# Kernel tuning notes

Measured on AMD Instinct MI355X. Metric: run time of the kernel, lower is better.

The kernel has to match this reference:

```python
import jax, jax.numpy as jnp
import numpy as np

B, H, L, D, S = 4, 16, 4096, 64, 128

def setup_inputs() -> dict:
    key = jax.random.key(0)
    k1, k2 = jax.random.split(key)
    x = jax.random.normal(k1, (B, H, L, D), dtype=jnp.float32)
    c = jax.random.normal(k2, (H, S, D), dtype=jnp.float32)
    # codebook rows are unit-normalized at init (matches torch init)
    c = c / jnp.linalg.norm(c, axis=-1, keepdims=True)
    return {"x": x, "c": c}

def reference(x, c):
    # cosine-similarity scores: [B,H,L,S]
    cos_sim = jnp.einsum('bhld,hsd->bhls', x, c)
    delta_index = jnp.argmax(cos_sim, axis=-1)            # [B,H,L]
    delta_onehot = jax.nn.one_hot(delta_index, c.shape[-2], dtype=jnp.float32)  # [B,H,L,S]
    return (delta_onehot, c)
```

## Files before the change

kernel.cpp:

```cpp
#include <hip/hip_runtime.h>
#include <hip/hip_bf16.h>
#include <math.h>

constexpr int BB = 4;
constexpr int HH = 16;
constexpr int LL = 4096;
constexpr int DD = 64;
constexpr int SS = 128;

constexpr int BM = 128;
constexpr int PP = 17;

__global__ __launch_bounds__(256) void quantizer_kernel(
    const float* __restrict__ x,
    const float* __restrict__ c,
    float* __restrict__ out,
    float* __restrict__ out_c)
{
    __shared__ float xs[DD * BM];
    __shared__ float cs[DD * SS];
    __shared__ int amax[BM];

    const int tid = threadIdx.x;
    const int blk = blockIdx.x;
    const long long r0 = (long long)blk * BM;
    const int h = (int)((r0 >> 12) & (HH - 1));
    const float* __restrict__ chead = c + (size_t)h * SS * DD;

    {
        const float4* __restrict__ xg = (const float4*)(x + (size_t)r0 * DD);
        const float4* __restrict__ cg = (const float4*)chead;
        #pragma unroll
        for (int it = 0; it < 8; ++it) {
            const int idx = tid + it * 256;
            const int row = idx & 127;
            const int d4  = idx >> 7;
            float4 v = xg[row * 16 + d4];
            xs[(4 * d4 + 0) * BM + row] = v.x;
            xs[(4 * d4 + 1) * BM + row] = v.y;
            xs[(4 * d4 + 2) * BM + row] = v.z;
            xs[(4 * d4 + 3) * BM + row] = v.w;
            float4 w = cg[row * 16 + d4];
            cs[(4 * d4 + 0) * SS + row] = w.x;
            cs[(4 * d4 + 1) * SS + row] = w.y;
            cs[(4 * d4 + 2) * SS + row] = w.z;
            cs[(4 * d4 + 3) * SS + row] = w.w;
        }
    }
    __syncthreads();

    const int m0 = tid >> 4;
    const int n0 = tid & 15;

    float acc[8][8] = {};

    #pragma unroll 2
    for (int k = 0; k < DD; ++k) {
        const float4 xa = *(const float4*)&xs[k * BM + m0 * 8];
        const float4 xb = *(const float4*)&xs[k * BM + m0 * 8 + 4];
        const float4 ca = *(const float4*)&cs[k * SS + n0 * 8];
        const float4 cb = *(const float4*)&cs[k * SS + n0 * 8 + 4];
        const float xv[8] = {xa.x, xa.y, xa.z, xa.w, xb.x, xb.y, xb.z, xb.w};
        const float cv[8] = {ca.x, ca.y, ca.z, ca.w, cb.x, cb.y, cb.z, cb.w};
        #pragma unroll
        for (int i = 0; i < 8; ++i)
            #pragma unroll
            for (int j = 0; j < 8; ++j)
                acc[i][j] = fmaf(xv[i], cv[j], acc[i][j]);
    }

    __syncthreads();
    float* pval = xs;
    int*   pidx = (int*)(xs + BM * PP);

    #pragma unroll
    for (int i = 0; i < 8; ++i) {
        float bv = acc[i][0];
        int bj = 0;
        #pragma unroll
        for (int j = 1; j < 8; ++j)
            if (acc[i][j] > bv) { bv = acc[i][j]; bj = j; }
        const int row = m0 * 8 + i;
        pval[row * PP + n0] = bv;
        pidx[row * PP + n0] = n0 * 8 + bj;
    }
    __syncthreads();

    if (tid < BM) {
        float bv = pval[tid * PP];
        int bi = pidx[tid * PP];
        #pragma unroll
        for (int t = 1; t < 16; ++t) {
            const float v = pval[tid * PP + t];
            const int ix = pidx[tid * PP + t];
            if (v > bv) { bv = v; bi = ix; }
        }
        amax[tid] = bi;
    }
    __syncthreads();

    float4* __restrict__ op = (float4*)(out + (size_t)r0 * SS);
    #pragma unroll 4
    for (int i = tid; i < BM * (SS / 4); i += 256) {
        const int rr = i >> 5;
        const int s0 = (i & 31) * 4;
        const int am = amax[rr];
        float4 v;
        v.x = (s0 + 0 == am) ? 1.f : 0.f;
        v.y = (s0 + 1 == am) ? 1.f : 0.f;
        v.z = (s0 + 2 == am) ? 1.f : 0.f;
        v.w = (s0 + 3 == am) ? 1.f : 0.f;
        op[i] = v;
    }

    if (blk < 128) {
        const float4* __restrict__ src = (const float4*)c;
        float4* __restrict__ dst = (float4*)out_c;
        const int idx = blk * 256 + tid;
        dst[idx] = src[idx];
    }
}

extern "C" void kernel_launch(void* const* d_in, const int* in_sizes, int n_in,
                              void* d_out, int out_size, void* d_ws, size_t ws_size,
                              hipStream_t stream) {
    const float* x = (const float*)d_in[0];
    const float* c = (const float*)d_in[1];
    float* out = (float*)d_out;
    float* out_c = out + (size_t)BB * HH * LL * SS;

    const int rows = BB * HH * LL;
    const int blocks = rows / BM;
    quantizer_kernel<<<blocks, 256, 0, stream>>>(x, c, out, out_c);
}
```

Before: 209.0 us.

## Use split-bf16 MFMA for scores with exact fp32 fallback for near ties

Replaces the fp32 FMA outer-product GEMM with bf16 MFMA 16x16x32. Each operand is split into a high and a low bf16 part and three cross products are summed to approximate fp32. Each row tracks its top-2 scores. Rows whose margin falls below a tolerance are flagged and rescored exactly in fp32 from global memory, which preserves argmax correctness. This offloads the compute to matrix cores, but adds a swizzled LDS layout, conversion overhead, and a serial per-flagged-row fallback loop with block-wide syncs.

```diff
diff --git a/kernel.cpp b/kernel.cpp
--- a/kernel.cpp
+++ b/kernel.cpp
@@ -1,5 +1,4 @@
 #include <hip/hip_runtime.h>
-#include <hip/hip_bf16.h>
 #include <math.h>
 
 constexpr int BB = 4;
@@ -7,9 +6,31 @@
 constexpr int LL = 4096;
 constexpr int DD = 64;
 constexpr int SS = 128;
-
 constexpr int BM = 128;
-constexpr int PP = 17;
+
+constexpr float TAU = 2e-3f;
+
+typedef __attribute__((ext_vector_type(8))) short bf16x8;
+typedef __attribute__((ext_vector_type(4))) float f32x4;
+
+#define MFMA16 __builtin_amdgcn_mfma_f32_16x16x32_bf16
+
+__device__ __forceinline__ unsigned short f2bf(float v) {
+    unsigned u = __float_as_uint(v);
+    return (unsigned short)((u + 0x7fffu + ((u >> 16) & 1u)) >> 16);
+}
+__device__ __forceinline__ float bf2f(unsigned short b) {
+    return __uint_as_float(((unsigned)b) << 16);
+}
+__device__ __forceinline__ unsigned swz(unsigned a) {
+    return a ^ (((a >> 8) & 3u) << 5);
+}
+__device__ __forceinline__ void st8(unsigned char* s, unsigned a, uint2 d) {
+    *(uint2*)(s + swz(a)) = d;
+}
+__device__ __forceinline__ bf16x8 ld8(const unsigned char* s, unsigned a) {
+    return *(const bf16x8*)(s + swz(a));
+}
 
 __global__ __launch_bounds__(256) void quantizer_kernel(
     const float* __restrict__ x,
@@ -17,9 +38,11 @@
     float* __restrict__ out,
     float* __restrict__ out_c)
 {
-    __shared__ float xs[DD * BM];
-    __shared__ float cs[DD * SS];
+    __shared__ __align__(16) unsigned char smem[65536];
     __shared__ int amax[BM];
+    __shared__ int s_nflag;
+    __shared__ int s_flag[BM];
+    __shared__ float s_fsc[SS];
 
     const int tid = threadIdx.x;
     const int blk = blockIdx.x;
@@ -27,77 +50,164 @@
     const int h = (int)((r0 >> 12) & (HH - 1));
     const float* __restrict__ chead = c + (size_t)h * SS * DD;
 
+    if (tid == 0) s_nflag = 0;
+
     {
         const float4* __restrict__ xg = (const float4*)(x + (size_t)r0 * DD);
         const float4* __restrict__ cg = (const float4*)chead;
         #pragma unroll
         for (int it = 0; it < 8; ++it) {
-            const int idx = tid + it * 256;
-            const int row = idx & 127;
-            const int d4  = idx >> 7;
-            float4 v = xg[row * 16 + d4];
-            xs[(4 * d4 + 0) * BM + row] = v.x;
-            xs[(4 * d4 + 1) * BM + row] = v.y;
-            xs[(4 * d4 + 2) * BM + row] = v.z;
-            xs[(4 * d4 + 3) * BM + row] = v.w;
-            float4 w = cg[row * 16 + d4];
-            cs[(4 * d4 + 0) * SS + row] = w.x;
-            cs[(4 * d4 + 1) * SS + row] = w.y;
-            cs[(4 * d4 + 2) * SS + row] = w.z;
-            cs[(4 * d4 + 3) * SS + row] = w.w;
+            const int idx = it * 256 + tid;
+            const int d4  = idx & 15;
+            const int row = idx >> 4;
+            const int kt  = d4 >> 3;
+            const int lsl = ((((d4 & 7) >> 1) << 4) | (row & 15));
+            const int boff = (d4 & 1) * 8;
+            const int t8  = row >> 4;
+            const unsigned bhi =
+                (unsigned)((((kt << 3) | t8) << 10) + lsl * 16 + boff);
+            const unsigned blo = bhi + (16u << 10);
+            {
+                float4 v = xg[idx];
+                unsigned short h0 = f2bf(v.x), h1 = f2bf(v.y),
+                               h2 = f2bf(v.z), h3 = f2bf(v.w);
+                unsigned short l0 = f2bf(v.x - bf2f(h0)),
+                               l1 = f2bf(v.y - bf2f(h1)),
+                               l2 = f2bf(v.z - bf2f(h2)),
+                               l3 = f2bf(v.w - bf2f(h3));
+                st8(smem, bhi, make_uint2((unsigned)h0 | ((unsigned)h1 << 16),
+                                          (unsigned)h2 | ((unsigned)h3 << 16)));
+                st8(smem, blo, make_uint2((unsigned)l0 | ((unsigned)l1 << 16),
+                                          (unsigned)l2 | ((unsigned)l3 << 16)));
+            }
+            {
+                float4 v = cg[idx];
+                unsigned short h0 = f2bf(v.x), h1 = f2bf(v.y),
+                               h2 = f2bf(v.z), h3 = f2bf(v.w);
+                unsigned short l0 = f2bf(v.x - bf2f(h0)),
+                               l1 = f2bf(v.y - bf2f(h1)),
+                               l2 = f2bf(v.z - bf2f(h2)),
+                               l3 = f2bf(v.w - bf2f(h3));
+                st8(smem, 32768u + bhi,
+                    make_uint2((unsigned)h0 | ((unsigned)h1 << 16),
+                               (unsigned)h2 | ((unsigned)h3 << 16)));
+                st8(smem, 32768u + blo,
+                    make_uint2((unsigned)l0 | ((unsigned)l1 << 16),
+                               (unsigned)l2 | ((unsigned)l3 << 16)));
+            }
         }
     }
     __syncthreads();
 
-    const int m0 = tid >> 4;
-    const int n0 = tid & 15;
-
-    float acc[8][8] = {};
-
-    #pragma unroll 2
-    for (int k = 0; k < DD; ++k) {
-        const float4 xa = *(const float4*)&xs[k * BM + m0 * 8];
-        const float4 xb = *(const float4*)&xs[k * BM + m0 * 8 + 4];
-        const float4 ca = *(const float4*)&cs[k * SS + n0 * 8];
-        const float4 cb = *(const float4*)&cs[k * SS + n0 * 8 + 4];
-        const float xv[8] = {xa.x, xa.y, xa.z, xa.w, xb.x, xb.y, xb.z, xb.w};
-        const float cv[8] = {ca.x, ca.y, ca.z, ca.w, cb.x, cb.y, cb.z, cb.w};
-        #pragma unroll
-        for (int i = 0; i < 8; ++i)
-            #pragma unroll
-            for (int j = 0; j < 8; ++j)
-                acc[i][j] = fmaf(xv[i], cv[j], acc[i][j]);
-    }
-
+    const int wv = tid >> 6;
+    const int lane = tid & 63;
+    const int ln15 = lane & 15;
+
+    bf16x8 af[2][2][2];
+    #pragma unroll
+    for (int rtb = 0; rtb < 2; ++rtb)
+        #pragma unroll
+        for (int kt = 0; kt < 2; ++kt)
+            #pragma unroll
+            for (int sp = 0; sp < 2; ++sp)
+                af[rtb][kt][sp] = ld8(smem,
+                    (unsigned)((((sp << 4) | (kt << 3) | (2 * wv + rtb)) << 10)
+                               + lane * 16));
+
+    float m1[2][4], m2[2][4];
+    int   mi_[2][4];
+    #pragma unroll
+    for (int rtb = 0; rtb < 2; ++rtb)
+        #pragma unroll
+        for (int r = 0; r < 4; ++r) {
+            m1[rtb][r] = -INFINITY; m2[rtb][r] = -INFINITY; mi_[rtb][r] = 0;
+        }
+
+    #pragma unroll
+    for (int ct = 0; ct < 8; ++ct) {
+        const unsigned bb = 32768u + (unsigned)(ct << 10) + (unsigned)(lane * 16);
+        bf16x8 b10 = ld8(smem, bb);
+        bf16x8 b11 = ld8(smem, bb + (1u << 13));
+        bf16x8 b20 = ld8(smem, bb + (1u << 14));
+        bf16x8 b21 = ld8(smem, bb + (1u << 14) + (1u << 13));
+        #pragma unroll
+        for (int rtb = 0; rtb < 2; ++rtb) {
+            f32x4 acc = {0.f, 0.f, 0.f, 0.f};
+            acc = MFMA16(af[rtb][0][1], b10, acc, 0, 0, 0);
+            acc = MFMA16(af[rtb][1][1], b11, acc, 0, 0, 0);
+            acc = MFMA16(af[rtb][0][0], b20, acc, 0, 0, 0);
+            acc = MFMA16(af[rtb][1][0], b21, acc, 0, 0, 0);
+            acc = MFMA16(af[rtb][0][0], b10, acc, 0, 0, 0);
+            acc = MFMA16(af[rtb][1][0], b11, acc, 0, 0, 0);
+            #pragma unroll
+            for (int r = 0; r < 4; ++r) {
+                const float v = acc[r];
+                const int col = ct * 16 + ln15;
+                if (v > m1[rtb][r]) {
+                    m2[rtb][r] = m1[rtb][r]; m1[rtb][r] = v; mi_[rtb][r] = col;
+                } else {
+                    m2[rtb][r] = fmaxf(m2[rtb][r], v);
+                }
+            }
+        }
+    }
+
+    #pragma unroll
+    for (int rtb = 0; rtb < 2; ++rtb) {
+        #pragma unroll
+        for (int r = 0; r < 4; ++r) {
+            float a1 = m1[rtb][r], a2 = m2[rtb][r];
+            int ai = mi_[rtb][r];
+            #pragma unroll
+            for (int off = 1; off <= 8; off <<= 1) {
+                const float o1 = __shfl_xor(a1, off);
+                const float o2 = __shfl_xor(a2, off);
+                const int   oi = __shfl_xor(ai, off);
+                const bool take = (o1 > a1) || (o1 == a1 && oi < ai);
+                const float n2 = take ? fmaxf(a1, o2) : fmaxf(a2, o1);
+                if (take) { a1 = o1; ai = oi; }
+                a2 = n2;
+            }
+            if (ln15 == 0) {
+                const int row = (2 * wv + rtb) * 16 + (lane >> 4) * 4 + r;
+                if (a1 - a2 >= TAU) {
+                    amax[row] = ai;
+                } else {
+                    const int p = atomicAdd(&s_nflag, 1);
+                    s_flag[p] = row;
+                }
+            }
+        }
+    }
     __syncthreads();
-    float* pval = xs;
-    int*   pidx = (int*)(xs + BM * PP);
-
-    #pragma unroll
-    for (int i = 0; i < 8; ++i) {
-        float bv = acc[i][0];
-        int bj = 0;
-        #pragma unroll
-        for (int j = 1; j < 8; ++j)
-            if (acc[i][j] > bv) { bv = acc[i][j]; bj = j; }
-        const int row = m0 * 8 + i;
-        pval[row * PP + n0] = bv;
-        pidx[row * PP + n0] = n0 * 8 + bj;
-    }
-    __syncthreads();
-
-    if (tid < BM) {
-        float bv = pval[tid * PP];
-        int bi = pidx[tid * PP];
-        #pragma unroll
-        for (int t = 1; t < 16; ++t) {
-            const float v = pval[tid * PP + t];
-            const int ix = pidx[tid * PP + t];
-            if (v > bv) { bv = v; bi = ix; }
-        }
-        amax[tid] = bi;
-    }
-    __syncthreads();
+
+    const int nf = s_nflag;
+    for (int f = 0; f < nf; ++f) {
+        const int row = s_flag[f];
+        if (tid < SS) {
+            const float4* __restrict__ xr =
+                (const float4*)(x + (size_t)(r0 + row) * DD);
+            const float4* __restrict__ cr =
+                (const float4*)(chead + (size_t)tid * DD);
+            float sc = 0.f;
+            #pragma unroll
+            for (int q = 0; q < 16; ++q) {
+                const float4 a = xr[q];
+                const float4 b = cr[q];
+                sc = fmaf(a.x, b.x, sc); sc = fmaf(a.y, b.y, sc);
+                sc = fmaf(a.z, b.z, sc); sc = fmaf(a.w, b.w, sc);
+            }
+            s_fsc[tid] = sc;
+        }
+        __syncthreads();
+        if (tid == 0) {
+            float bv = s_fsc[0]; int bi = 0;
+            for (int s = 1; s < SS; ++s)
+                if (s_fsc[s] > bv) { bv = s_fsc[s]; bi = s; }
+            amax[row] = bi;
+        }
+        __syncthreads();
+    }
 
     float4* __restrict__ op = (float4*)(out + (size_t)r0 * SS);
     #pragma unroll 4
```

Measured after the change: 216.1 us. 1.03x slower.
